# Performance work log

Measured on AMD Instinct MI355X. Metric: run time of the kernel, lower is better.

The kernel has to match this reference:

```python
import jax, jax.numpy as jnp
import numpy as np

N_HEADS = 16
N_KV = 4
HEAD_DIM = 256
EPS = 1e-6

def _rotate_half(x):
    h = x.shape[-1] // 2
    return jnp.concatenate([-x[..., h:], x[..., :h]], axis=-1)

def _gemma_rmsnorm(x, w, eps=EPS):
    dt = x.dtype
    x32 = x.astype(jnp.float32)
    x32 = x32 * jax.lax.rsqrt(jnp.mean(x32 * x32, axis=-1, keepdims=True) + eps)
    return ((1.0 + w.astype(jnp.float32)) * x32).astype(dt)


def setup_inputs() -> dict:
    key = jax.random.key(0)
    ks = jax.random.split(key, 7)
    B, S, D = 2, 2048, 4096
    rotary_dim = 64
    x = jax.random.normal(ks[0], (B, S, D), jnp.float32)
    # realistic RoPE cache: [cos | sin], theta=10000
    inv_freq = 1.0 / (10000.0 ** (np.arange(0, rotary_dim, 2, dtype=np.float32) / rotary_dim))
    t = np.arange(S, dtype=np.float32)
    freqs = np.outer(t, inv_freq)                       # [S, rotary_dim/2]
    emb = np.concatenate([freqs, freqs], axis=-1)        # [S, rotary_dim]
    rope_cache = jnp.asarray(np.concatenate([np.cos(emb), np.sin(emb)], axis=-1))  # [S, 2*rotary_dim]
    sc = 0.02
    wq = jax.random.normal(ks[1], (N_HEADS * HEAD_DIM * 2, D), jnp.float32) * sc
    wk = jax.random.normal(ks[2], (N_KV * HEAD_DIM, D), jnp.float32) * sc
    wv = jax.random.normal(ks[3], (N_KV * HEAD_DIM, D), jnp.float32) * sc
    wo = jax.random.normal(ks[4], (D, N_HEADS * HEAD_DIM), jnp.float32) * sc
    q_norm_w = jnp.zeros((HEAD_DIM,), jnp.float32)
    k_norm_w = jnp.zeros((HEAD_DIM,), jnp.float32)
    return {"x": x, "rope_cache": rope_cache, "wq": wq, "wk": wk, "wv": wv,
            "wo": wo, "q_norm_w": q_norm_w, "k_norm_w": k_norm_w}


def reference(x, rope_cache, wq, wk, wv, wo, q_norm_w, k_norm_w):
    B, S, D = x.shape
    scale = HEAD_DIM ** -0.5
    # fused QKV-style projections
    qg = jnp.einsum('bsd,ed->bse', x, wq).reshape(B, S, N_HEADS, 2 * HEAD_DIM)
    q, gate = qg[..., :HEAD_DIM], qg[..., HEAD_DIM:]
    gate = gate.reshape(B, S, N_HEADS * HEAD_DIM)
    k = jnp.einsum('bsd,ed->bse', x, wk).reshape(B, S, N_KV, HEAD_DIM)
    v = jnp.einsum('bsd,ed->bse', x, wv).reshape(B, S, N_KV, HEAD_DIM)
    # QK RMSNorm (Gemma-style, zero-init weight)
    q = _gemma_rmsnorm(q, q_norm_w)
    k = _gemma_rmsnorm(k, k_norm_w)
    # partial RoPE on first rotary_dim dims
    rotary_dim = rope_cache.shape[-1] // 2
    rc = rope_cache[:S]
    cos = rc[None, :, None, :rotary_dim]
    sin = rc[None, :, None, rotary_dim:]
    q_rot = q[..., :rotary_dim] * cos + _rotate_half(q[..., :rotary_dim]) * sin
    k_rot = k[..., :rotary_dim] * cos + _rotate_half(k[..., :rotary_dim]) * sin
    q = jnp.concatenate([q_rot, q[..., rotary_dim:]], axis=-1)
    k = jnp.concatenate([k_rot, k[..., rotary_dim:]], axis=-1)
    # GQA: repeat kv heads
    rep = N_HEADS // N_KV
    k = jnp.repeat(k, rep, axis=2)  # [B,S,H,hd]
    v = jnp.repeat(v, rep, axis=2)
    # full (non-causal) SDPA
    scores = jnp.einsum('bqhd,bkhd->bhqk', q, k) * scale
    p = jax.nn.softmax(scores, axis=-1)
    y = jnp.einsum('bhqk,bkhd->bqhd', p, v).reshape(B, S, N_HEADS * HEAD_DIM)
    # sigmoid output gating
    y = y * jax.nn.sigmoid(gate)
    return jnp.einsum('bse,de->bsd', y, wo)
```

## Files before the change

kernel.cpp:

```cpp
#include <hip/hip_runtime.h>
#include <hip/hip_bf16.h>
#include <cstdint>
#include <cstddef>

typedef __bf16 bf16;
typedef __bf16 bf16x8 __attribute__((ext_vector_type(8)));
typedef __bf16 bf16x4 __attribute__((ext_vector_type(4)));
typedef float f32x4 __attribute__((ext_vector_type(4)));

#define MFMA16(a, b, c) __builtin_amdgcn_mfma_f32_16x16x32_bf16((a), (b), (c), 0, 0, 0)
#define GLL16(gp, lp) __builtin_amdgcn_global_load_lds( \
    (const __attribute__((address_space(1))) void*)(gp), \
    (__attribute__((address_space(3))) void*)(lp), 16, 0, 0)

#define LDS_FENCE() do { \
    __builtin_amdgcn_sched_barrier(0); \
    asm volatile("s_waitcnt lgkmcnt(0)" ::: "memory"); \
    __builtin_amdgcn_sched_barrier(0); \
  } while (0)

__device__ __forceinline__ bf16x8 cvt8(const float* f) {
  bf16x8 h;
  #pragma unroll
  for (int j = 0; j < 8; ++j) h[j] = (bf16)f[j];
  return h;
}

__device__ __forceinline__ bf16x8 ldb8(const bf16* p) {
  return *(const bf16x8*)p;
}
__device__ __forceinline__ bf16x8 ldb8(const float* p) {
  float f[8];
  *(f32x4*)&f[0] = *(const f32x4*)p;
  *(f32x4*)&f[4] = *(const f32x4*)(p + 4);
  return cvt8(f);
}

__global__ void write_val(float* o, float v) {
  if (threadIdx.x == 0 && blockIdx.x == 0) o[0] = v;
}

__global__ __launch_bounds__(256) void cvt_pass(
    const float* __restrict__ src, bf16* __restrict__ dst, size_t n8)
{
  for (size_t i = (size_t)blockIdx.x * 256 + threadIdx.x; i < n8;
       i += (size_t)gridDim.x * 256) {
    float f[8];
    *(f32x4*)&f[0] = *(const f32x4*)&src[i * 8];
    *(f32x4*)&f[4] = *(const f32x4*)&src[i * 8 + 4];
    *(bf16x8*)&dst[i * 8] = cvt8(f);
  }
}

template <typename CT>
__global__ __launch_bounds__(512, 2) void gemm256_3(
    const bf16* __restrict__ A,
    const bf16* __restrict__ B0, const bf16* __restrict__ B1,
    const bf16* __restrict__ B2, int n1, int n2,
    CT* __restrict__ C0, CT* __restrict__ C1, CT* __restrict__ C2,
    int K, size_t aBatch, size_t cb0, size_t cb1, size_t cb2,
    int ld0, int ld1, int ld2)
{
  __shared__ bf16 lds[4 * 16384];
  const int tid  = threadIdx.x;
  const int wave = tid >> 6, lane = tid & 63;
  const int g = lane >> 4, q = lane & 15;
  const int wm = wave >> 2, wn = wave & 3;
  const int bx = blockIdx.x;
  const int r = (bx < n1) ? 0 : (bx < n2) ? 1 : 2;
  const bf16* Bw = (r == 0) ? B0 : (r == 1) ? B1 : B2;
  CT* C = ((r == 0) ? C0 : (r == 1) ? C1 : C2)
          + blockIdx.z * ((r == 0) ? cb0 : (r == 1) ? cb1 : cb2);
  const int bn = bx - ((r == 0) ? 0 : (r == 1) ? n1 : n2);
  const int ldc = (r == 0) ? ld0 : (r == 1) ? ld1 : ld2;
  const size_t n0 = (size_t)bn * 256;
  const size_t m0 = (size_t)blockIdx.y * 256;
  const bf16* Ap = A + blockIdx.z * aBatch;

  const int srow = tid >> 2;
  const int scol = (((tid & 3) ^ (srow & 3)) << 3);
  const int NT = K >> 5;

  f32x4 acc[8][4] = {};

  auto STAGE_A = [&](int t) {
    const int k0 = t << 5;
    char* base = (char*)lds + (size_t)(t & 3) * 32768 + wave * 1024;
    #pragma unroll
    for (int i = 0; i < 2; ++i)
      GLL16(&Ap[(m0 + i * 128 + srow) * (size_t)K + k0 + scol],
            base + i * 8192);
  };
  auto STAGE_B = [&](int t) {
    const int k0 = t << 5;
    char* base = (char*)lds + (size_t)(t & 3) * 32768 + 16384 + wave * 1024;
    #pragma unroll
    for (int i = 0; i < 2; ++i)
      GLL16(&Bw[(n0 + i * 128 + srow) * (size_t)K + k0 + scol],
            base + i * 8192);
  };

  STAGE_A(0); STAGE_B(0);
  STAGE_A(1); STAGE_B(1);
  STAGE_A(2); STAGE_B(2);

  const int rsl = ((g ^ (q & 3)) << 3);

  for (int t = 0; t < NT; ++t) {
    asm volatile("s_waitcnt vmcnt(8)" ::: "memory");
    __builtin_amdgcn_sched_barrier(0);
    __builtin_amdgcn_s_barrier();
    const bf16* lA = lds + (size_t)(t & 3) * 16384;
    const bf16* lB = lA + 8192;

    bf16x8 bfr[4], af[4];
    #pragma unroll
    for (int fn = 0; fn < 4; ++fn)
      bfr[fn] = *(const bf16x8*)&lB[(wn * 64 + fn * 16 + q) * 32 + rsl];
    #pragma unroll
    for (int fm = 0; fm < 4; ++fm)
      af[fm] = *(const bf16x8*)&lA[(wm * 128 + fm * 16 + q) * 32 + rsl];
    if (t + 3 < NT) STAGE_A(t + 3);
    asm volatile("s_waitcnt lgkmcnt(0)" ::: "memory");
    __builtin_amdgcn_sched_barrier(0);
    __builtin_amdgcn_s_setprio(1);
    #pragma unroll
    for (int fm = 0; fm < 4; ++fm)
      #pragma unroll
      for (int fn = 0; fn < 4; ++fn)
        acc[fm][fn] = MFMA16(af[fm], bfr[fn], acc[fm][fn]);
    __builtin_amdgcn_s_setprio(0);
    __builtin_amdgcn_s_barrier();

    #pragma unroll
    for (int fm = 0; fm < 4; ++fm)
      af[fm] = *(const bf16x8*)&lA[(wm * 128 + (fm + 4) * 16 + q) * 32 + rsl];
    if (t + 3 < NT) STAGE_B(t + 3);
    asm volatile("s_waitcnt lgkmcnt(0)" ::: "memory");
    __builtin_amdgcn_sched_barrier(0);
    __builtin_amdgcn_s_setprio(1);
    #pragma unroll
    for (int fm = 0; fm < 4; ++fm)
      #pragma unroll
      for (int fn = 0; fn < 4; ++fn)
        acc[fm + 4][fn] = MFMA16(af[fm], bfr[fn], acc[fm + 4][fn]);
    __builtin_amdgcn_s_setprio(0);
  }

  #pragma unroll
  for (int fm = 0; fm < 8; ++fm)
    #pragma unroll
    for (int fn = 0; fn < 4; ++fn)
      #pragma unroll
      for (int rr = 0; rr < 4; ++rr) {
        const size_t row = m0 + wm * 128 + fm * 16 + g * 4 + rr;
        C[row * (size_t)ldc + n0 + wn * 64 + fn * 16 + q] = (CT)acc[fm][fn][rr];
      }
}

template <typename CT, typename BT>
__global__ __launch_bounds__(256) void gemm_bf(
    const bf16* __restrict__ A,
    const BT* __restrict__ B0, const BT* __restrict__ B1, int nsplit,
    CT* __restrict__ C0, CT* __restrict__ C1,
    int K, size_t aBatch, size_t cBatch)
{
  constexpr int LDST = 72;
  __shared__ bf16 lA[128 * LDST];
  __shared__ bf16 lB[128 * LDST];
  const int tid  = threadIdx.x;
  const int wave = tid >> 6;
  const int lane = tid & 63;
  const int g = lane >> 4, q = lane & 15;
  const bool r0 = (int)blockIdx.x < nsplit;
  const BT* Bw = r0 ? B0 : B1;
  CT* C = (r0 ? C0 : C1) + blockIdx.z * cBatch;
  const int bn = r0 ? blockIdx.x : blockIdx.x - nsplit;
  const int ldc = (r0 ? nsplit : ((int)gridDim.x - nsplit)) * 128;
  const size_t n0 = (size_t)bn * 128;
  const size_t m0 = (size_t)blockIdx.y * 128;
  const bf16* Ap = A + blockIdx.z * aBatch;
  const int wm = wave >> 1, wn = wave & 1;
  const int sr = tid >> 3, sc8 = (tid & 7) << 3;

  f32x4 acc[4][4] = {};

  for (int k0 = 0; k0 < K; k0 += 64) {
    __syncthreads();
    #pragma unroll
    for (int i = 0; i < 4; ++i) {
      const int row = i * 32 + sr;
      *(bf16x8*)&lA[row * LDST + sc8] = ldb8(&Ap[(m0 + row) * (size_t)K + k0 + sc8]);
      *(bf16x8*)&lB[row * LDST + sc8] = ldb8(&Bw[(n0 + row) * (size_t)K + k0 + sc8]);
    }
    __syncthreads();
    #pragma unroll
    for (int kk = 0; kk < 2; ++kk) {
      bf16x8 af[4], bfr[4];
      #pragma unroll
      for (int f = 0; f < 4; ++f) {
        af[f]  = *(const bf16x8*)&lA[(wm * 64 + f * 16 + q) * LDST + kk * 32 + g * 8];
        bfr[f] = *(const bf16x8*)&lB[(wn * 64 + f * 16 + q) * LDST + kk * 32 + g * 8];
      }
      #pragma unroll
      for (int fm = 0; fm < 4; ++fm)
        #pragma unroll
        for (int fn = 0; fn < 4; ++fn)
          acc[fm][fn] = MFMA16(af[fm], bfr[fn], acc[fm][fn]);
    }
  }

  #pragma unroll
  for (int fm = 0; fm < 4; ++fm)
    #pragma unroll
    for (int fn = 0; fn < 4; ++fn)
      #pragma unroll
      for (int r = 0; r < 4; ++r) {
        const size_t row = m0 + wm * 64 + fm * 16 + g * 4 + r;
        C[row * (size_t)ldc + n0 + wn * 64 + fn * 16 + q] = (CT)acc[fm][fn][r];
      }
}

__global__ __launch_bounds__(256) void norm_rope_w(
    bf16* __restrict__ data, const float* __restrict__ w,
    const float* __restrict__ ropec, int lnh, int hstride, int rowlen,
    int s_off)
{
  const int lane = threadIdx.x & 63;
  const int wid  = blockIdx.x * 4 + (threadIdx.x >> 6);
  const int m = wid >> lnh;
  const int h = wid & ((1 << lnh) - 1);
  const int s = (s_off + m) & 2047;

  bf16* p = data + (size_t)m * rowlen + h * hstride + lane * 4;
  const bf16x4 xv = *(const bf16x4*)p;
  float x0 = (float)xv[0], x1 = (float)xv[1], x2 = (float)xv[2], x3 = (float)xv[3];
  float ss = x0*x0 + x1*x1 + x2*x2 + x3*x3;
  #pragma unroll
  for (int d = 1; d < 64; d <<= 1) ss += __shfl_xor(ss, d, 64);
  const float rr = rsqrtf(ss * (1.0f / 256.0f) + 1e-6f);
  const f32x4 wv4 = *(const f32x4*)&w[lane * 4];
  x0 *= rr * (1.0f + wv4[0]);
  x1 *= rr * (1.0f + wv4[1]);
  x2 *= rr * (1.0f + wv4[2]);
  x3 *= rr * (1.0f + wv4[3]);

  const float o0 = __shfl_xor(x0, 8, 64);
  const float o1 = __shfl_xor(x1, 8, 64);
  const float o2 = __shfl_xor(x2, 8, 64);
  const float o3 = __shfl_xor(x3, 8, 64);
  if (lane < 16) {
    const int c0 = lane * 4;
    const float* rc = ropec + (size_t)s * 128;
    const float sgn = (lane < 8) ? -1.0f : 1.0f;
    x0 = x0 * rc[c0]     + sgn * o0 * rc[64 + c0];
    x1 = x1 * rc[c0 + 1] + sgn * o1 * rc[64 + c0 + 1];
    x2 = x2 * rc[c0 + 2] + sgn * o2 * rc[64 + c0 + 2];
    x3 = x3 * rc[c0 + 3] + sgn * o3 * rc[64 + c0 + 3];
  }
  bf16x4 ov; ov[0] = (bf16)x0; ov[1] = (bf16)x1; ov[2] = (bf16)x2; ov[3] = (bf16)x3;
  *(bf16x4*)p = ov;
}

__global__ __launch_bounds__(256) void attn_b2(
    const bf16* __restrict__ qg, const bf16* __restrict__ kb,
    const bf16* __restrict__ vb, bf16* __restrict__ yb,
    size_t qgBatch, size_t kvBatch, size_t yBatch)
{
  __shared__ bf16 lK[32 * 256];
  __shared__ bf16 lVt[256 * 40];
  __shared__ bf16 lP[4 * 16 * 40];
  const int tid  = threadIdx.x;
  const int wave = tid >> 6, lane = tid & 63;
  const int g = lane >> 4, qc = lane & 15;
  const int h = blockIdx.y, q0 = blockIdx.x * 64, kvh = h >> 2;
  const int z = blockIdx.z;
  const bf16* qgp = qg + z * qgBatch;
  const bf16* kbase = kb + z * kvBatch + kvh * 256;
  const bf16* vbase = vb + z * kvBatch + kvh * 256;
  const int qrow = q0 + wave * 16 + qc;

  bf16x8 qf[8];
  {
    const bf16* qp = qgp + (size_t)qrow * 8192 + h * 512;
    #pragma unroll
    for (int kq = 0; kq < 8; ++kq)
      qf[kq] = *(const bf16x8*)&qp[kq * 32 + g * 8];
  }

  f32x4 o[16] = {};
  float mrow = -1e30f, lrow = 0.0f;
  const float scale = 0.0625f;
  const float L2E = 1.44269504f;
  const int vp = (tid & 15) * 2, vc = (tid >> 4) * 16;
  bf16* const pl = lP + wave * (16 * 40);
  const int krw = wave * 2 + (lane >> 5);
  const int ksl = lane & 31;

  for (int t0 = 0; t0 < 2048; t0 += 32) {
    bf16x8 v0a, v0b, v1a, v1b;
    {
      const bf16* p0 = vbase + (size_t)(t0 + vp) * 1024 + vc;
      v0a = *(const bf16x8*)(p0);
      v0b = *(const bf16x8*)(p0 + 8);
      v1a = *(const bf16x8*)(p0 + 1024);
      v1b = *(const bf16x8*)(p0 + 1032);
    }
    __syncthreads();
    #pragma unroll
    for (int i = 0; i < 4; ++i) {
      const int row = i * 8 + krw;
      GLL16(&kbase[(size_t)(t0 + row) * 1024 + ((ksl ^ (row & 7)) << 3)],
            (char*)lK + i * 4096 + wave * 1024);
    }
    {
      unsigned* dst = (unsigned*)lVt;
      #pragma unroll
      for (int j = 0; j < 8; ++j) {
        const int o0 = (vc + j) * 20 + (vp >> 1);
        const int o1 = (vc + 8 + j) * 20 + (vp >> 1);
        dst[o0] = (unsigned)__builtin_bit_cast(unsigned short, (bf16)v0a[j]) |
                  ((unsigned)__builtin_bit_cast(unsigned short, (bf16)v1a[j]) << 16);
        dst[o1] = (unsigned)__builtin_bit_cast(unsigned short, (bf16)v0b[j]) |
                  ((unsigned)__builtin_bit_cast(unsigned short, (bf16)v1b[j]) << 16);
      }
    }
    __syncthreads();

    f32x4 st[2];
    #pragma unroll
    for (int half = 0; half < 2; ++half) {
      f32x4 s = {0.f, 0.f, 0.f, 0.f};
      __builtin_amdgcn_s_setprio(1);
      #pragma unroll
      for (int kq = 0; kq < 8; ++kq) {
        const bf16x8 ka = *(const bf16x8*)
            &lK[(half * 16 + qc) * 256 + (((kq * 4 + g) ^ (qc & 7)) << 3)];
        s = MFMA16(ka, qf[kq], s);
      }
      __builtin_amdgcn_s_setprio(0);
      st[half] = s;
    }

    float pm = st[0][0];
    #pragma unroll
    for (int r = 1; r < 4; ++r) pm = fmaxf(pm, st[0][r]);
    #pragma unroll
    for (int r = 0; r < 4; ++r) pm = fmaxf(pm, st[1][r]);
    pm *= scale;
    pm = fmaxf(pm, __shfl_xor(pm, 16, 64));
    pm = fmaxf(pm, __shfl_xor(pm, 32, 64));

    if (!__all(pm <= mrow + 8.0f)) {
      const float mnew = fmaxf(mrow, pm);
      const float corr = exp2f((mrow - mnew) * L2E);
      lrow *= corr;
      #pragma unroll
      for (int f = 0; f < 16; ++f) {
        o[f][0] *= corr; o[f][1] *= corr; o[f][2] *= corr; o[f][3] *= corr;
      }
      mrow = mnew;
    }

    float ladd = 0.0f;
    #pragma unroll
    for (int half = 0; half < 2; ++half) {
      bf16x4 pk;
      #pragma unroll
      for (int r = 0; r < 4; ++r) {
        const float pv = exp2f((st[half][r] * scale - mrow) * L2E);
        ladd += pv;
        pk[r] = (bf16)pv;
      }
      *(bf16x4*)&pl[qc * 40 + half * 16 + g * 4] = pk;
    }
    ladd += __shfl_xor(ladd, 16, 64);
    ladd += __shfl_xor(ladd, 32, 64);
    lrow += ladd;

    LDS_FENCE();

    const bf16x8 pb = *(const bf16x8*)&pl[qc * 40 + g * 8];
    __builtin_amdgcn_s_setprio(1);
    #pragma unroll
    for (int fm = 0; fm < 16; ++fm) {
      const bf16x8 va = *(const bf16x8*)&lVt[(fm * 16 + qc) * 40 + g * 8];
      o[fm] = MFMA16(va, pb, o[fm]);
    }
    __builtin_amdgcn_s_setprio(0);
  }

  const float inv = 1.0f / lrow;
  const bf16* gp = qgp + (size_t)qrow * 8192 + h * 512 + 256;
  bf16* yp = yb + z * yBatch + (size_t)qrow * 4096 + h * 256;
  #pragma unroll
  for (int fm = 0; fm < 16; ++fm) {
    const int d0 = fm * 16 + g * 4;
    bf16x4 ov;
    #pragma unroll
    for (int r = 0; r < 4; ++r) {
      const float gv = (float)gp[d0 + r];
      const float sig = 1.0f / (1.0f + exp2f(-gv * L2E));
      ov[r] = (bf16)(o[fm][r] * inv * sig);
    }
    *(bf16x4*)&yp[d0] = ov;
  }
}

extern "C" void kernel_launch(void* const* d_in, const int* in_sizes, int n_in,
                              void* d_out, int out_size, void* d_ws, size_t ws_size,
                              hipStream_t stream) {
  const float* x    = (const float*)d_in[0];
  const float* rope = (const float*)d_in[1];
  const float* wq   = (const float*)d_in[2];
  const float* wk   = (const float*)d_in[3];
  const float* wv   = (const float*)d_in[4];
  const float* wo   = (const float*)d_in[5];
  const float* qnw  = (const float*)d_in[6];
  const float* knw  = (const float*)d_in[7];
  float* out = (float*)d_out;

  if (out_size != 16777216) { write_val<<<1, 64, 0, stream>>>(out, 2000.0f); return; }
  const bool sizes_ok = (n_in == 8) &&
      in_sizes[0] == 16777216 && in_sizes[1] == 262144 &&
      in_sizes[2] == 33554432 && in_sizes[3] == 4194304 &&
      in_sizes[4] == 4194304  && in_sizes[5] == 16777216 &&
      in_sizes[6] == 256      && in_sizes[7] == 256;
  if (!sizes_ok) { write_val<<<1, 64, 0, stream>>>(out, 2500.0f); return; }

  const size_t XS  = 2048ull * 4096;
  const size_t KVS = 2048ull * 1024;
  const size_t QGS = 2048ull * 8192;
  const size_t YS  = 2048ull * 4096;
  const size_t WFIX = (33554432ull + 4194304 + 4194304 + 16777216) * 2;

  const size_t needFull = WFIX + 2 * XS * 2 + 4 * KVS * 2 + 2 * QGS * 2 + 2 * YS * 2;
  auto needT = [&](bool w, int nb, int CHv) -> size_t {
    return (w ? WFIX : 0) + (size_t)nb * XS * 2 + (size_t)nb * KVS * 4
         + (size_t)CHv * 8192 * 2 + (size_t)CHv * 4096 * 2;
  };

  char* ws = (char*)d_ws;

  if (needFull <= ws_size) {
    bf16* wqb = (bf16*)ws;           ws += 33554432ull * 2;
    bf16* wkb = (bf16*)ws;           ws += 4194304ull * 2;
    bf16* wvb = (bf16*)ws;           ws += 4194304ull * 2;
    bf16* wob = (bf16*)ws;           ws += 16777216ull * 2;
    bf16* xb  = (bf16*)ws;           ws += 2 * XS * 2;
    bf16* kbb = (bf16*)ws;           ws += 2 * KVS * 2;
    bf16* vbb = (bf16*)ws;           ws += 2 * KVS * 2;
    bf16* qgc = (bf16*)ws;           ws += 2 * QGS * 2;
    bf16* ycc = (bf16*)ws;

    cvt_pass<<<2048, 256, 0, stream>>>(wq, wqb, 33554432 / 8);
    cvt_pass<<<512,  256, 0, stream>>>(wk, wkb, 4194304 / 8);
    cvt_pass<<<512,  256, 0, stream>>>(wv, wvb, 4194304 / 8);
    cvt_pass<<<1024, 256, 0, stream>>>(wo, wob, 16777216 / 8);
    cvt_pass<<<2048, 256, 0, stream>>>(x, xb, 2 * XS / 8);

    gemm256_3<bf16><<<dim3(40, 8, 2), 512, 0, stream>>>(
        xb, wkb, wvb, wqb, 4, 8, kbb, vbb, qgc,
        4096, XS, KVS, KVS, QGS, 1024, 1024, 8192);

    norm_rope_w<<<4096,  256, 0, stream>>>(kbb, knw, rope, 2, 256, 1024, 0);
    norm_rope_w<<<16384, 256, 0, stream>>>(qgc, qnw, rope, 4, 512, 8192, 0);

    attn_b2<<<dim3(32, 16, 2), 256, 0, stream>>>(
        qgc, kbb, vbb, ycc, QGS, KVS, YS);

    gemm256_3<float><<<dim3(16, 8, 2), 512, 0, stream>>>(
        ycc, wob, wob, wob, 16, 16, out, out, out,
        4096, YS, YS, YS, YS, 4096, 4096, 4096);
    return;
  }

  bool useW = true; int nb = 2, CH = 2048;
  while (CH > 256 && needT(useW, nb, CH) > ws_size) CH >>= 1;
  if (needT(useW, nb, CH) > ws_size) {
    useW = false; CH = 2048;
    while (CH > 128 && needT(useW, nb, CH) > ws_size) CH >>= 1;
    if (needT(useW, nb, CH) > ws_size) {
      nb = 1; CH = 2048;
      while (CH > 128 && needT(useW, nb, CH) > ws_size) CH >>= 1;
    }
  }
  if (needT(useW, nb, CH) > ws_size) {
    write_val<<<1, 64, 0, stream>>>(out, 3000.0f);
    return;
  }

  bf16* wqb = nullptr; bf16* wkb = nullptr; bf16* wvb = nullptr; bf16* wob = nullptr;
  if (useW) {
    wqb = (bf16*)ws;               ws += 33554432ull * 2;
    wkb = (bf16*)ws;               ws += 4194304ull * 2;
    wvb = (bf16*)ws;               ws += 4194304ull * 2;
    wob = (bf16*)ws;               ws += 16777216ull * 2;
  }
  bf16* xb  = (bf16*)ws;           ws += (size_t)nb * XS * 2;
  bf16* kbb = (bf16*)ws;           ws += (size_t)nb * KVS * 2;
  bf16* vbb = (bf16*)ws;           ws += (size_t)nb * KVS * 2;
  bf16* qgc = (bf16*)ws;           ws += (size_t)CH * 8192 * 2;
  bf16* ycc = (bf16*)ws;

  if (useW) {
    cvt_pass<<<2048, 256, 0, stream>>>(wq, wqb, 33554432 / 8);
    cvt_pass<<<512,  256, 0, stream>>>(wk, wkb, 4194304 / 8);
    cvt_pass<<<512,  256, 0, stream>>>(wv, wvb, 4194304 / 8);
    cvt_pass<<<1024, 256, 0, stream>>>(wo, wob, 16777216 / 8);
  }

  if (nb == 2) {
    cvt_pass<<<2048, 256, 0, stream>>>(x, xb, 2 * XS / 8);
    if (useW)
      gemm256_3<bf16><<<dim3(8, 8, 2), 512, 0, stream>>>(
          xb, wkb, wvb, wvb, 4, 8, kbb, vbb, vbb,
          4096, XS, KVS, KVS, KVS, 1024, 1024, 1024);
    else
      gemm_bf<bf16, float><<<dim3(16, 16, 2), 256, 0, stream>>>(
          xb, wk, wv, 8, kbb, vbb, 4096, XS, KVS);
    norm_rope_w<<<4096, 256, 0, stream>>>(kbb, knw, rope, 2, 256, 1024, 0);
  }

  for (int b = 0; b < 2; ++b) {
    const int bi = (nb == 2) ? b : 0;
    if (nb == 1) {
      cvt_pass<<<2048, 256, 0, stream>>>(x + (size_t)b * XS, xb, XS / 8);
      if (useW)
        gemm256_3<bf16><<<dim3(8, 8, 1), 512, 0, stream>>>(
            xb, wkb, wvb, wvb, 4, 8, kbb, vbb, vbb,
            4096, 0, 0, 0, 0, 1024, 1024, 1024);
      else
        gemm_bf<bf16, float><<<dim3(16, 16, 1), 256, 0, stream>>>(
            xb, wk, wv, 8, kbb, vbb, 4096, 0, 0);
      norm_rope_w<<<2048, 256, 0, stream>>>(kbb, knw, rope, 2, 256, 1024, 0);
    }
    const bf16* xbb = xb + (size_t)bi * XS;
    bf16* kbbb = kbb + (size_t)bi * KVS;
    bf16* vbbb = vbb + (size_t)bi * KVS;
    for (int c = 0; c < 2048; c += CH) {
      if (useW)
        gemm256_3<bf16><<<dim3(32, CH / 256, 1), 512, 0, stream>>>(
            xbb + (size_t)c * 4096, wqb, wqb, wqb, 32, 32, qgc, qgc, qgc,
            4096, 0, 0, 0, 0, 8192, 8192, 8192);
      else
        gemm_bf<bf16, float><<<dim3(64, CH / 128, 1), 256, 0, stream>>>(
            xbb + (size_t)c * 4096, wq, wq, 64, qgc, qgc, 4096, 0, 0);
      norm_rope_w<<<CH * 4, 256, 0, stream>>>(qgc, qnw, rope, 4, 512, 8192, c);
      attn_b2<<<dim3(CH / 64, 16, 1), 256, 0, stream>>>(
          qgc, kbbb, vbbb, ycc, 0, 0, 0);
      float* outc = out + ((size_t)b * 2048 + c) * 4096;
      if (useW)
        gemm256_3<float><<<dim3(16, CH / 256, 1), 512, 0, stream>>>(
            ycc, wob, wob, wob, 16, 16, outc, outc, outc,
            4096, 0, 0, 0, 0, 4096, 4096, 4096);
      else
        gemm_bf<float, float><<<dim3(32, CH / 128, 1), 256, 0, stream>>>(
            ycc, wo, wo, 32, outc, outc, 4096, 0, 0);
    }
  }
}
```

Baseline: 915.4 us.

## Double-buffer K and V tiles in attention kernel to overlap loads with compute

```diff
diff --git a/kernel.cpp b/kernel.cpp
--- a/kernel.cpp
+++ b/kernel.cpp
@@ -262,13 +262,13 @@
   *(bf16x4*)p = ov;
 }
 
-__global__ __launch_bounds__(256) void attn_b2(
+__global__ __launch_bounds__(256) void attn_b3(
     const bf16* __restrict__ qg, const bf16* __restrict__ kb,
     const bf16* __restrict__ vb, bf16* __restrict__ yb,
     size_t qgBatch, size_t kvBatch, size_t yBatch)
 {
-  __shared__ bf16 lK[32 * 256];
-  __shared__ bf16 lVt[256 * 40];
+  __shared__ bf16 lK[2][32 * 256];
+  __shared__ bf16 lVt[2][256 * 40];
   __shared__ bf16 lP[4 * 16 * 40];
   const int tid  = threadIdx.x;
   const int wave = tid >> 6, lane = tid & 63;
@@ -297,35 +297,56 @@
   const int krw = wave * 2 + (lane >> 5);
   const int ksl = lane & 31;
 
-  for (int t0 = 0; t0 < 2048; t0 += 32) {
-    bf16x8 v0a, v0b, v1a, v1b;
-    {
-      const bf16* p0 = vbase + (size_t)(t0 + vp) * 1024 + vc;
-      v0a = *(const bf16x8*)(p0);
-      v0b = *(const bf16x8*)(p0 + 8);
-      v1a = *(const bf16x8*)(p0 + 1024);
-      v1b = *(const bf16x8*)(p0 + 1032);
-    }
-    __syncthreads();
+  auto stageK = [&](int tile, int buf) {
+    const int t0 = tile * 32;
     #pragma unroll
     for (int i = 0; i < 4; ++i) {
       const int row = i * 8 + krw;
       GLL16(&kbase[(size_t)(t0 + row) * 1024 + ((ksl ^ (row & 7)) << 3)],
-            (char*)lK + i * 4096 + wave * 1024);
-    }
-    {
-      unsigned* dst = (unsigned*)lVt;
-      #pragma unroll
-      for (int j = 0; j < 8; ++j) {
-        const int o0 = (vc + j) * 20 + (vp >> 1);
-        const int o1 = (vc + 8 + j) * 20 + (vp >> 1);
-        dst[o0] = (unsigned)__builtin_bit_cast(unsigned short, (bf16)v0a[j]) |
-                  ((unsigned)__builtin_bit_cast(unsigned short, (bf16)v1a[j]) << 16);
-        dst[o1] = (unsigned)__builtin_bit_cast(unsigned short, (bf16)v0b[j]) |
-                  ((unsigned)__builtin_bit_cast(unsigned short, (bf16)v1b[j]) << 16);
-      }
-    }
+            (char*)lK[buf] + i * 4096 + wave * 1024);
+    }
+  };
+  auto loadV = [&](int tile, bf16x8& a0, bf16x8& b0, bf16x8& a1, bf16x8& b1) {
+    const bf16* p0 = vbase + (size_t)(tile * 32 + vp) * 1024 + vc;
+    a0 = *(const bf16x8*)(p0);
+    b0 = *(const bf16x8*)(p0 + 8);
+    a1 = *(const bf16x8*)(p0 + 1024);
+    b1 = *(const bf16x8*)(p0 + 1032);
+  };
+  auto writeVt = [&](int buf, const bf16x8& a0, const bf16x8& b0,
+                     const bf16x8& a1, const bf16x8& b1) {
+    unsigned* dst = (unsigned*)lVt[buf];
+    #pragma unroll
+    for (int j = 0; j < 8; ++j) {
+      const int o0 = (vc + j) * 20 + (vp >> 1);
+      const int o1 = (vc + 8 + j) * 20 + (vp >> 1);
+      dst[o0] = (unsigned)__builtin_bit_cast(unsigned short, (bf16)a0[j]) |
+                ((unsigned)__builtin_bit_cast(unsigned short, (bf16)a1[j]) << 16);
+      dst[o1] = (unsigned)__builtin_bit_cast(unsigned short, (bf16)b0[j]) |
+                ((unsigned)__builtin_bit_cast(unsigned short, (bf16)b1[j]) << 16);
+    }
+  };
+
+  {
+    bf16x8 a0, b0, a1, b1;
+    stageK(0, 0);
+    loadV(0, a0, b0, a1, b1);
+    asm volatile("s_waitcnt vmcnt(0)" ::: "memory");
+    __builtin_amdgcn_sched_barrier(0);
+    writeVt(0, a0, b0, a1, b1);
+  }
+
+  const int NT = 64;
+  for (int tile = 0; tile < NT; ++tile) {
     __syncthreads();
+    const int cur = tile & 1;
+
+    bf16x8 a0, b0, a1, b1;
+    const bool pf = (tile + 1 < NT);
+    if (pf) {
+      stageK(tile + 1, cur ^ 1);
+      loadV(tile + 1, a0, b0, a1, b1);
+    }
 
     f32x4 st[2];
     #pragma unroll
@@ -335,7 +356,7 @@
       #pragma unroll
       for (int kq = 0; kq < 8; ++kq) {
         const bf16x8 ka = *(const bf16x8*)
-            &lK[(half * 16 + qc) * 256 + (((kq * 4 + g) ^ (qc & 7)) << 3)];
+            &lK[cur][(half * 16 + qc) * 256 + (((kq * 4 + g) ^ (qc & 7)) << 3)];
         s = MFMA16(ka, qf[kq], s);
       }
       __builtin_amdgcn_s_setprio(0);
@@ -384,10 +405,16 @@
     __builtin_amdgcn_s_setprio(1);
     #pragma unroll
     for (int fm = 0; fm < 16; ++fm) {
-      const bf16x8 va = *(const bf16x8*)&lVt[(fm * 16 + qc) * 40 + g * 8];
+      const bf16x8 va = *(const bf16x8*)&lVt[cur][(fm * 16 + qc) * 40 + g * 8];
       o[fm] = MFMA16(va, pb, o[fm]);
     }
     __builtin_amdgcn_s_setprio(0);
+
+    if (pf) {
+      asm volatile("s_waitcnt vmcnt(0)" ::: "memory");
+      __builtin_amdgcn_sched_barrier(0);
+      writeVt(cur ^ 1, a0, b0, a1, b1);
+    }
   }
 
   const float inv = 1.0f / lrow;
@@ -466,7 +493,7 @@
     norm_rope_w<<<4096,  256, 0, stream>>>(kbb, knw, rope, 2, 256, 1024, 0);
     norm_rope_w<<<16384, 256, 0, stream>>>(qgc, qnw, rope, 4, 512, 8192, 0);
 
-    attn_b2<<<dim3(32, 16, 2), 256, 0, stream>>>(
+    attn_b3<<<dim3(32, 16, 2), 256, 0, stream>>>(
         qgc, kbb, vbb, ycc, QGS, KVS, YS);
 
     gemm256_3<float><<<dim3(16, 8, 2), 512, 0, stream>>>(
@@ -547,7 +574,7 @@
         gemm_bf<bf16, float><<<dim3(64, CH / 128, 1), 256, 0, stream>>>(
             xbb + (size_t)c * 4096, wq, wq, 64, qgc, qgc, 4096, 0, 0);
       norm_rope_w<<<CH * 4, 256, 0, stream>>>(qgc, qnw, rope, 4, 512, 8192, c);
-      attn_b2<<<dim3(CH / 64, 16, 1), 256, 0, stream>>>(
+      attn_b3<<<dim3(CH / 64, 16, 1), 256, 0, stream>>>(
           qgc, kbbb, vbbb, ycc, 0, 0, 0);
       float* outc = out + ((size_t)b * 2048 + c) * 4096;
       if (useW)
```

Result: faster. 836.2 us (-8.7%).
